# Optimization experiments

Hardware: AMD Instinct MI355X
Metric: run time of the kernel (lower is better)

## Reference

```python
import jax, jax.numpy as jnp
import numpy as np

EPS = 1e-08


def setup_inputs() -> dict:
    key = jax.random.key(0)
    k1, k2, k3 = jax.random.split(key, 3)
    N, IN_DIM, OUT_DIM = 8192, 512, 512
    h = jax.random.normal(k1, (N, IN_DIM), dtype=jnp.float32)
    adj = jax.random.randint(k2, (N, N), 0, 2, dtype=jnp.int32)
    # nn.Linear(in_dim, out_dim, bias=False) weight: [out_dim, in_dim]
    W = jax.random.normal(k3, (OUT_DIM, IN_DIM), dtype=jnp.float32) * (1.0 / np.sqrt(IN_DIM))
    return {"h": h, "adj": adj, "W": W}


def reference(h, adj, W):
    # Wh = h @ W^T  -> [N, out_dim]
    Wh = h @ W.T
    N = Wh.shape[0]
    norms = jnp.linalg.norm(Wh, axis=1, keepdims=True)  # [N, 1]
    # cosine similarity [N, N]
    sim = (Wh @ Wh.T) / (norms * norms.T + EPS)
    mask = (adj > 0) | jnp.eye(N, dtype=bool)
    sim_masked = jnp.where(mask, sim, -jnp.inf)
    alpha = jax.nn.softmax(sim_masked, axis=1)
    return alpha @ Wh
```

## Files before the change

kernel.cpp:

```cpp
#include <hip/hip_runtime.h>
#include <hip/hip_bf16.h>
#include <stdint.h>

#define NN 8192
#define DD 512

typedef unsigned short u16;
typedef __attribute__((ext_vector_type(8))) short short8;
typedef __attribute__((ext_vector_type(4))) float f32x4;

__device__ __forceinline__ void gld_lds16(const void* g, void* l) {
  __builtin_amdgcn_global_load_lds(
      (const __attribute__((address_space(1))) uint32_t*)(uintptr_t)g,
      (__attribute__((address_space(3))) uint32_t*)(uintptr_t)l,
      16, 0, 0);
}

__device__ __forceinline__ u16 f2bf(float f) {
  __hip_bfloat16 b = __float2bfloat16(f);
  return __builtin_bit_cast(u16, b);
}

__global__ void fill_kernel(float* __restrict__ p, int n, float v) {
  int i = blockIdx.x * 256 + threadIdx.x;
  int stride = gridDim.x * 256;
  for (; i < n; i += stride) p[i] = v;
}

__global__ void cvt4_kernel(const float4* __restrict__ src, ushort4* __restrict__ dst, int n4) {
  int i = blockIdx.x * 256 + threadIdx.x;
  int stride = gridDim.x * 256;
  for (; i < n4; i += stride) {
    float4 v = src[i];
    ushort4 o;
    o.x = f2bf(v.x); o.y = f2bf(v.y); o.z = f2bf(v.z); o.w = f2bf(v.w);
    dst[i] = o;
  }
}

__global__ void rownorm_kernel(const float* __restrict__ Wh, float* __restrict__ invn,
                               float* __restrict__ den) {
  int row = blockIdx.x;
  int l = threadIdx.x;
  const float4* p = (const float4*)(Wh + (size_t)row * DD);
  float4 a = p[l], b = p[l + 64];
  float s = a.x*a.x + a.y*a.y + a.z*a.z + a.w*a.w
          + b.x*b.x + b.y*b.y + b.z*b.z + b.w*b.w;
  #pragma unroll
  for (int off = 32; off; off >>= 1) s += __shfl_down(s, off);
  if (l == 0) {
    invn[row] = 1.0f / sqrtf(s);
    den[row] = 0.0f;
  }
}

__global__ void u_wht_kernel(const float* __restrict__ Wh, const float* __restrict__ invn,
                             u16* __restrict__ U, u16* __restrict__ WhT) {
  __shared__ float tile[64][65];
  int i0 = blockIdx.x * 64, d0 = blockIdx.y * 64;
  int c = threadIdx.x & 63, rb = threadIdx.x >> 6;
  #pragma unroll
  for (int r = rb; r < 64; r += 4) {
    float v = Wh[(size_t)(i0 + r) * DD + d0 + c];
    tile[r][c] = v;
    U[(size_t)(i0 + r) * DD + d0 + c] = f2bf(v * invn[i0 + r]);
  }
  __syncthreads();
  #pragma unroll
  for (int r = rb; r < 64; r += 4) {
    WhT[(size_t)(d0 + r) * NN + i0 + c] = f2bf(tile[c][r]);
  }
}

__global__ void __launch_bounds__(256) gemm_wh(
    const u16* __restrict__ A, const u16* __restrict__ B,
    int Nn, int K, float* __restrict__ Cf)
{
  __shared__ __align__(16) u16 As[128 * 32];
  __shared__ __align__(16) u16 Bs[128 * 32];

  const int tid = threadIdx.x;
  const int w = tid >> 6;
  const int lane = tid & 63;
  const int lm = lane & 15;
  const int q = lane >> 4;
  const int row0 = blockIdx.y * 128;
  const int col0 = blockIdx.x * 128;
  const int RM = (w >> 1) * 64;
  const int RN = (w & 1) * 64;
  const int sr = tid >> 2;
  const int sk = (tid & 3) * 8;

  f32x4 acc[4][4];
  #pragma unroll
  for (int a_ = 0; a_ < 4; a_++)
    #pragma unroll
    for (int b_ = 0; b_ < 4; b_++)
      acc[a_][b_] = (f32x4){0.f, 0.f, 0.f, 0.f};

  const size_t Abase = (size_t)row0 * K;
  const size_t Bbase = (size_t)col0 * K;

  for (int k0 = 0; k0 < K; k0 += 32) {
    __syncthreads();
    gld_lds16(A + Abase + (size_t)sr * K + k0 + sk,        (char*)As + w * 1024);
    gld_lds16(A + Abase + (size_t)(sr + 64) * K + k0 + sk, (char*)As + 4096 + w * 1024);
    gld_lds16(B + Bbase + (size_t)sr * K + k0 + sk,        (char*)Bs + w * 1024);
    gld_lds16(B + Bbase + (size_t)(sr + 64) * K + k0 + sk, (char*)Bs + 4096 + w * 1024);
    __syncthreads();

    short8 af[4], bfr[4];
    #pragma unroll
    for (int mt = 0; mt < 4; mt++)
      af[mt] = *(const short8*)&As[(RM + mt * 16 + lm) * 32 + q * 8];
    #pragma unroll
    for (int nt = 0; nt < 4; nt++)
      bfr[nt] = *(const short8*)&Bs[(RN + nt * 16 + lm) * 32 + q * 8];

    #pragma unroll
    for (int mt = 0; mt < 4; mt++)
      #pragma unroll
      for (int nt = 0; nt < 4; nt++)
        acc[mt][nt] = __builtin_amdgcn_mfma_f32_16x16x32_bf16(af[mt], bfr[nt], acc[mt][nt], 0, 0, 0);
  }

  #pragma unroll
  for (int mt = 0; mt < 4; mt++) {
    const int ib = row0 + RM + mt * 16 + q * 4;
    #pragma unroll
    for (int rr = 0; rr < 4; rr++) {
      const int i = ib + rr;
      #pragma unroll
      for (int nt = 0; nt < 4; nt++) {
        const int jc = col0 + RN + nt * 16 + lm;
        Cf[(size_t)i * Nn + jc] = acc[mt][nt][rr];
      }
    }
  }
}

__global__ void __launch_bounds__(512, 4) gemm_sim(
    const u16* __restrict__ U, const int* __restrict__ adj,
    u16* __restrict__ Pb, float* __restrict__ den)
{
  __shared__ __align__(16) char lds[49152];

  const int bj = blockIdx.x;
  const int bi = blockIdx.y;

  const int tid = threadIdx.x;
  const int w = tid >> 6;
  const int lane = tid & 63;
  const int lm = lane & 15;
  const int q = lane >> 4;
  const int row0 = bi * 256;
  const int col0 = bj * 128;
  const int wm = w >> 1;
  const int wn = w & 1;

  const u16* Ab = U + (size_t)row0 * DD;
  const u16* Bb = U + (size_t)col0 * DD;

  const int srow = tid >> 2;
  const int sch8 = (((tid & 3) ^ ((tid >> 3) & 3)) << 3);
  const int wofs = w << 10;

  const int rA = wm * 64 + lm;
  const int rB = wn * 64 + lm;
  const int aoff = rA * 64 + ((q ^ ((rA >> 1) & 3)) << 4);
  const int boff = 16384 + rB * 64 + ((q ^ ((rB >> 1) & 3)) << 4);

  f32x4 acc[4][4];
  #pragma unroll
  for (int a_ = 0; a_ < 4; a_++)
    #pragma unroll
    for (int b_ = 0; b_ < 4; b_++)
      acc[a_][b_] = (f32x4){0.f, 0.f, 0.f, 0.f};

  int na0[4][4], na1[4][4];
  {
    const int ib0 = row0 + wm * 64 + q * 4;
    #pragma unroll
    for (int rr = 0; rr < 4; rr++)
      #pragma unroll
      for (int nt = 0; nt < 4; nt++)
        na0[rr][nt] = adj[(size_t)(ib0 + rr) * NN + col0 + wn * 64 + nt * 16 + lm];
  }
  asm volatile("" ::: "memory");

#define SSTAGE(koff, dstoff)                                                      \
  do {                                                                            \
    char* d_ = lds + (dstoff);                                                    \
    gld_lds16(Ab + (size_t)srow * DD + (koff) + sch8,         d_ + wofs);         \
    gld_lds16(Ab + (size_t)(srow + 128) * DD + (koff) + sch8, d_ + 8192 + wofs);  \
    gld_lds16(Bb + (size_t)srow * DD + (koff) + sch8,         d_ + 16384 + wofs); \
  } while (0)

  SSTAGE(0, 0);
  SSTAGE(32, 24576);
  asm volatile("s_waitcnt vmcnt(3)" ::: "memory");
  asm volatile("s_barrier" ::: "memory");

#define STILE(T, CBOFF)                                                           \
  do {                                                                            \
    const char* cb = lds + (CBOFF);                                               \
    short8 af[4], bfr[4];                                                         \
    _Pragma("unroll")                                                             \
    for (int m = 0; m < 4; m++)                                                   \
      af[m] = *(const short8*)(cb + aoff + m * 1024);                             \
    _Pragma("unroll")                                                             \
    for (int n = 0; n < 4; n++)                                                   \
      bfr[n] = *(const short8*)(cb + boff + n * 1024);                            \
    asm volatile("s_barrier" ::: "memory");                                       \
    asm volatile("s_waitcnt lgkmcnt(0)" ::: "memory");                            \
    __builtin_amdgcn_s_setprio(1);                                                \
    _Pragma("unroll")                                                             \
    for (int m = 0; m < 2; m++)                                                   \
      _Pragma("unroll")                                                           \
      for (int n = 0; n < 4; n++)                                                 \
        acc[m][n] = __builtin_amdgcn_mfma_f32_16x16x32_bf16(af[m], bfr[n], acc[m][n], 0, 0, 0); \
    __builtin_amdgcn_s_setprio(0);                                                \
    asm volatile("s_barrier" ::: "memory");                                       \
    if ((T) + 2 < 16) SSTAGE(((T) + 2) * 32, CBOFF);                              \
    asm volatile("s_barrier" ::: "memory");                                       \
    __builtin_amdgcn_s_setprio(1);                                                \
    _Pragma("unroll")                                                             \
    for (int m = 2; m < 4; m++)                                                   \
      _Pragma("unroll")                                                           \
      for (int n = 0; n < 4; n++)                                                 \
        acc[m][n] = __builtin_amdgcn_mfma_f32_16x16x32_bf16(af[m], bfr[n], acc[m][n], 0, 0, 0); \
    __builtin_amdgcn_s_setprio(0);                                                \
    if ((T) + 2 < 16) { asm volatile("s_waitcnt vmcnt(3)" ::: "memory"); }        \
    else              { asm volatile("s_waitcnt vmcnt(0)" ::: "memory"); }        \
    asm volatile("s_barrier" ::: "memory");                                       \
  } while (0)

  #pragma unroll 1
  for (int t = 0; t < 16; t += 2) {
    STILE(t, 0);
    STILE(t + 1, 24576);
  }
#undef STILE
#undef SSTAGE

#define EPI(MT, NAC, NAN, DOLOAD)                                                 \
  do {                                                                            \
    if (DOLOAD) {                                                                 \
      const int ibn = row0 + wm * 64 + ((MT) + 1) * 16 + q * 4;                   \
      _Pragma("unroll")                                                           \
      for (int rr = 0; rr < 4; rr++)                                              \
        _Pragma("unroll")                                                         \
        for (int nt = 0; nt < 4; nt++)                                            \
          NAN[rr][nt] = adj[(size_t)(ibn + rr) * NN + col0 + wn * 64 + nt * 16 + lm]; \
    }                                                                             \
    const int ibc = row0 + wm * 64 + (MT) * 16 + q * 4;                           \
    _Pragma("unroll")                                                             \
    for (int rr = 0; rr < 4; rr++) {                                              \
      const int i = ibc + rr;                                                     \
      float psum = 0.f;                                                           \
      _Pragma("unroll")                                                           \
      for (int nt = 0; nt < 4; nt++) {                                            \
        const int jc = col0 + wn * 64 + nt * 16 + lm;                             \
        const float ev = __expf(acc[MT][nt][rr]);                                 \
        const bool on = (NAC[rr][nt] != 0) || (i == jc);                          \
        const float p = on ? ev : 0.0f;                                           \
        psum += p;                                                                \
        Pb[(size_t)i * NN + jc] = f2bf(p);                                        \
      }                                                                           \
      _Pragma("unroll")                                                           \
      for (int off = 8; off; off >>= 1) psum += __shfl_down(psum, off, 16);       \
      if (lm == 0) atomicAdd(&den[i], psum);                                      \
    }                                                                             \
  } while (0)

  EPI(0, na0, na1, 1);
  EPI(1, na1, na0, 1);
  EPI(2, na0, na1, 1);
  EPI(3, na1, na0, 0);
#undef EPI
}

__global__ void __launch_bounds__(512, 2) gemm_out2(
    const u16* __restrict__ P_,
    const u16* __restrict__ Wt,
    u16* __restrict__ p0, u16* __restrict__ p1,
    u16* __restrict__ p2, u16* __restrict__ p3)
{
  __shared__ __align__(16) char lds[65536];

  const int tid = threadIdx.x;
  const int lane = tid & 63;
  const int lm = lane & 15;
  const int q = lane >> 4;
  const int w = tid >> 6;
  const int wm = w >> 2;
  const int wn = w & 3;
  const int row0 = blockIdx.x * 256;
  const int col0 = blockIdx.y * 256;
  const int z = blockIdx.z;
  const int kBegin = z * (NN / 4);
  const int NT = (NN / 4) / 32;

  const u16* Ab = P_ + (size_t)row0 * NN;
  const u16* Bb = Wt + (size_t)col0 * NN;

  const int srow = tid >> 2;
  const int sch8 = (((tid & 3) ^ ((tid >> 3) & 3)) << 3);
  const int wofs = (tid >> 6) << 10;

  const int rA = wm * 128 + lm;
  const int rB = wn * 64 + lm;
  const int aoff = rA * 64 + ((q ^ ((rA >> 1) & 3)) << 4);
  const int boff = 16384 + rB * 64 + ((q ^ ((rB >> 1) & 3)) << 4);

  f32x4 acc[8][4];
  #pragma unroll
  for (int m = 0; m < 8; m++)
    #pragma unroll
    for (int n = 0; n < 4; n++)
      acc[m][n] = (f32x4){0.f, 0.f, 0.f, 0.f};

#define STAGE4(koff, dstoff)                                                      \
  do {                                                                            \
    char* d_ = lds + (dstoff);                                                    \
    gld_lds16(Ab + (size_t)srow * NN + (koff) + sch8,         d_ + wofs);         \
    gld_lds16(Ab + (size_t)(srow + 128) * NN + (koff) + sch8, d_ + 8192 + wofs);  \
    gld_lds16(Bb + (size_t)srow * NN + (koff) + sch8,         d_ + 16384 + wofs); \
    gld_lds16(Bb + (size_t)(srow + 128) * NN + (koff) + sch8, d_ + 24576 + wofs); \
  } while (0)

  STAGE4(kBegin, 0);
  STAGE4(kBegin + 32, 32768);
  asm volatile("s_waitcnt vmcnt(4)" ::: "memory");
  asm volatile("s_barrier" ::: "memory");

#define TILE(T, CBOFF)                                                            \
  do {                                                                            \
    const char* cb = lds + (CBOFF);                                               \
    short8 af[8], bf_[4];                                                         \
    _Pragma("unroll")                                                             \
    for (int m = 0; m < 8; m++)                                                   \
      af[m] = *(const short8*)(cb + aoff + m * 1024);                             \
    _Pragma("unroll")                                                             \
    for (int n = 0; n < 4; n++)                                                   \
      bf_[n] = *(const short8*)(cb + boff + n * 1024);                            \
    asm volatile("s_barrier" ::: "memory");                                       \
    asm volatile("s_waitcnt lgkmcnt(0)" ::: "memory");                            \
    __builtin_amdgcn_s_setprio(1);                                                \
    _Pragma("unroll")                                                             \
    for (int m = 0; m < 4; m++)                                                   \
      _Pragma("unroll")                                                           \
      for (int n = 0; n < 4; n++)                                                 \
        acc[m][n] = __builtin_amdgcn_mfma_f32_16x16x32_bf16(af[m], bf_[n], acc[m][n], 0, 0, 0); \
    __builtin_amdgcn_s_setprio(0);                                                \
    asm volatile("s_barrier" ::: "memory");                                       \
    if ((T) + 2 < NT) STAGE4(kBegin + ((T) + 2) * 32, CBOFF);                     \
    asm volatile("s_barrier" ::: "memory");                                       \
    __builtin_amdgcn_s_setprio(1);                                                \
    _Pragma("unroll")                                                             \
    for (int m = 4; m < 8; m++)                                                   \
      _Pragma("unroll")                                                           \
      for (int n = 0; n < 4; n++)                                                 \
        acc[m][n] = __builtin_amdgcn_mfma_f32_16x16x32_bf16(af[m], bf_[n], acc[m][n], 0, 0, 0); \
    __builtin_amdgcn_s_setprio(0);                                                \
    if ((T) + 2 < NT) { asm volatile("s_waitcnt vmcnt(4)" ::: "memory"); }        \
    else              { asm volatile("s_waitcnt vmcnt(0)" ::: "memory"); }        \
    asm volatile("s_barrier" ::: "memory");                                       \
  } while (0)

  #pragma unroll 1
  for (int t = 0; t < NT; t += 2) {
    TILE(t, 0);
    TILE(t + 1, 32768);
  }
#undef TILE
#undef STAGE4

  u16* const part = (z == 0) ? p0 : (z == 1) ? p1 : (z == 2) ? p2 : p3;
  #pragma unroll
  for (int m = 0; m < 8; m++) {
    const int ib = row0 + wm * 128 + m * 16 + q * 4;
    #pragma unroll
    for (int rr = 0; rr < 4; rr++) {
      const int i = ib + rr;
      #pragma unroll
      for (int n = 0; n < 4; n++) {
        const int dc = col0 + wn * 64 + n * 16 + lm;
        part[(size_t)i * DD + dc] = f2bf(acc[m][n][rr]);
      }
    }
  }
}

__global__ void reduce4_kernel(const uint4* __restrict__ p0, const uint4* __restrict__ p1,
                               const uint4* __restrict__ p2, const uint4* __restrict__ p3,
                               const float* __restrict__ den, float4* __restrict__ out) {
  const int idx = blockIdx.x * 256 + threadIdx.x;
  const int row = idx >> 6;
  const float dinv = 1.0f / den[row];
  float s[8] = {0, 0, 0, 0, 0, 0, 0, 0};
  #pragma unroll
  for (int zp = 0; zp < 4; zp++) {
    const uint4 u = (zp == 0 ? p0 : zp == 1 ? p1 : zp == 2 ? p2 : p3)[idx];
    s[0] += __uint_as_float(u.x << 16); s[1] += __uint_as_float(u.x & 0xffff0000u);
    s[2] += __uint_as_float(u.y << 16); s[3] += __uint_as_float(u.y & 0xffff0000u);
    s[4] += __uint_as_float(u.z << 16); s[5] += __uint_as_float(u.z & 0xffff0000u);
    s[6] += __uint_as_float(u.w << 16); s[7] += __uint_as_float(u.w & 0xffff0000u);
  }
  float4 o0 = {s[0] * dinv, s[1] * dinv, s[2] * dinv, s[3] * dinv};
  float4 o1 = {s[4] * dinv, s[5] * dinv, s[6] * dinv, s[7] * dinv};
  out[idx * 2] = o0;
  out[idx * 2 + 1] = o1;
}

extern "C" void kernel_launch(void* const* d_in, const int* in_sizes, int n_in,
                              void* d_out, int out_size, void* d_ws, size_t ws_size,
                              hipStream_t stream) {
  const float* h = (const float*)d_in[0];
  const int* adj = (const int*)d_in[1];
  const float* W = (const float*)d_in[2];
  float* out = (float*)d_out;

  const size_t SZ_P    = (size_t)NN * NN * 2;
  const size_t SZ_X0   = (size_t)NN * NN / 8;
  const size_t SZ_WHT  = (size_t)DD * NN * 2;
  const size_t SZ_HB   = (size_t)NN * DD * 2;
  const size_t SZ_WB   = (size_t)DD * DD * 2;
  const size_t SZ_U    = (size_t)NN * DD * 2;
  const size_t SZ_P3   = (size_t)NN * DD * 2;
  const size_t NEEDED  = SZ_P + SZ_X0 + SZ_WHT + SZ_HB + SZ_WB + SZ_U + SZ_P3 + 2 * (size_t)NN * 4;

  if (ws_size < NEEDED) {
    fill_kernel<<<256, 256, 0, stream>>>(out, out_size, 12345.0f);
    return;
  }

  char* ws = (char*)d_ws;
  size_t off = 0;
  u16*   P    = (u16*)(ws + off); off += SZ_P;
  u16*   x0   = (u16*)(ws + off); off += SZ_X0;
  u16*   WhT  = (u16*)(ws + off); off += SZ_WHT;
  u16*   hb   = (u16*)(ws + off); off += SZ_HB;
  u16*   Wb   = (u16*)(ws + off); off += SZ_WB;
  u16*   U    = (u16*)(ws + off); off += SZ_U;
  u16*   p3   = (u16*)(ws + off); off += SZ_P3;
  float* invn = (float*)(ws + off);
  float* den  = invn + NN;

  float* Wh = (float*)P;
  u16* part0 = x0;
  u16* part1 = U;
  u16* part2 = hb;
  u16* part3 = p3;

  cvt4_kernel<<<1024, 256, 0, stream>>>((const float4*)h, (ushort4*)hb, NN * DD / 4);
  cvt4_kernel<<<256, 256, 0, stream>>>((const float4*)W, (ushort4*)Wb, DD * DD / 4);
  gemm_wh<<<dim3(DD / 128, NN / 128), 256, 0, stream>>>(hb, Wb, DD, DD, Wh);
  rownorm_kernel<<<NN, 64, 0, stream>>>(Wh, invn, den);
  u_wht_kernel<<<dim3(NN / 64, DD / 64), 256, 0, stream>>>(Wh, invn, U, WhT);
  gemm_sim<<<dim3(NN / 128, NN / 256), 512, 0, stream>>>(U, adj, P, den);
  gemm_out2<<<dim3(NN / 256, DD / 256, 4), 512, 0, stream>>>(P, WhT, part0, part1, part2, part3);
  reduce4_kernel<<<NN * DD / 8 / 256, 256, 0, stream>>>(
      (const uint4*)part0, (const uint4*)part1, (const uint4*)part2, (const uint4*)part3,
      den, (float4*)out);
}
```

Measured before the change: 576.7 us.

## Fuse similarity, masking, exp and output GEMM into a flash-style kernel

Replaces the separate similarity GEMM (which wrote the full NxN bf16 probability matrix to global memory) and the split-K output GEMM with one flash-attention-style kernel. Each block keeps a 64-row Q tile in registers, streams K tiles and Wh^T tiles through LDS, computes exp with the adjacency mask into an LDS P tile, and accumulates P@Wh directly. The key range is split in two halves whose fp32 partials are summed by a lighter reduce kernel. This removes the large P round-trip through HBM, at the cost of a 144KB LDS footprint, high register pressure from 32 Q fragments held per thread, and only 256 blocks of occupancy.

```diff
diff --git a/kernel.cpp b/kernel.cpp
--- a/kernel.cpp
+++ b/kernel.cpp
@@ -139,278 +139,226 @@
   }
 }
 
-__global__ void __launch_bounds__(512, 4) gemm_sim(
-    const u16* __restrict__ U, const int* __restrict__ adj,
-    u16* __restrict__ Pb, float* __restrict__ den)
+__global__ void __launch_bounds__(512, 2) flash(
+    const u16* __restrict__ U,
+    const u16* __restrict__ Wt,
+    const int* __restrict__ adj,
+    float* __restrict__ accH,
+    float* __restrict__ den)
 {
-  __shared__ __align__(16) char lds[49152];
-
-  const int bj = blockIdx.x;
-  const int bi = blockIdx.y;
+  __shared__ __align__(16) char lds[147456];
+  constexpr int KV0 = 0, KV1 = 32768, WT0 = 65536, WT1 = 98304, POFF = 131072;
 
   const int tid = threadIdx.x;
   const int w = tid >> 6;
   const int lane = tid & 63;
   const int lm = lane & 15;
   const int q = lane >> 4;
-  const int row0 = bi * 256;
-  const int col0 = bj * 128;
-  const int wm = w >> 1;
-  const int wn = w & 1;
-
-  const u16* Ab = U + (size_t)row0 * DD;
-  const u16* Bb = U + (size_t)col0 * DD;
-
-  const int srow = tid >> 2;
-  const int sch8 = (((tid & 3) ^ ((tid >> 3) & 3)) << 3);
-  const int wofs = w << 10;
-
-  const int rA = wm * 64 + lm;
-  const int rB = wn * 64 + lm;
-  const int aoff = rA * 64 + ((q ^ ((rA >> 1) & 3)) << 4);
-  const int boff = 16384 + rB * 64 + ((q ^ ((rB >> 1) & 3)) << 4);
-
-  f32x4 acc[4][4];
-  #pragma unroll
-  for (int a_ = 0; a_ < 4; a_++)
-    #pragma unroll
-    for (int b_ = 0; b_ < 4; b_++)
-      acc[a_][b_] = (f32x4){0.f, 0.f, 0.f, 0.f};
-
-  int na0[4][4], na1[4][4];
+  const int rg = w >> 2;
+  const int xg = w & 3;
+  const int jh = blockIdx.x;
+  const int i0 = blockIdx.y * 64;
+  const int jb = jh * (NN / 2);
+  float* accP = accH + (size_t)jh * NN * DD;
+
+  const int kvrow = tid >> 4;
+  const int kvsrc = ((tid & 15) ^ (((tid >> 4) & 7) << 1)) * 8;
+  const int wtrow = tid >> 2;
+  const int wtsrc = ((tid & 3) ^ ((tid >> 3) & 3)) * 8;
+  const int sdst = w << 10;
+  const int sk_x = (lm & 7) << 1;
+  const int wq_x = (q ^ ((lm >> 1) & 3)) << 4;
+
+  f32x4 acc_s0[2], acc_s1[2], acc_o0[8], acc_o1[8];
+  #pragma unroll
+  for (int n = 0; n < 2; n++) { acc_s0[n] = (f32x4){0.f,0.f,0.f,0.f}; acc_s1[n] = (f32x4){0.f,0.f,0.f,0.f}; }
+  #pragma unroll
+  for (int n = 0; n < 8; n++) { acc_o0[n] = (f32x4){0.f,0.f,0.f,0.f}; acc_o1[n] = (f32x4){0.f,0.f,0.f,0.f}; }
+  float dacc0[4] = {0.f,0.f,0.f,0.f}, dacc1[4] = {0.f,0.f,0.f,0.f};
+  int na0[2][4], na1[2][4];
+
+  short8 Qf0[16], Qf1[16];
   {
-    const int ib0 = row0 + wm * 64 + q * 4;
-    #pragma unroll
-    for (int rr = 0; rr < 4; rr++)
-      #pragma unroll
-      for (int nt = 0; nt < 4; nt++)
-        na0[rr][nt] = adj[(size_t)(ib0 + rr) * NN + col0 + wn * 64 + nt * 16 + lm];
+    const u16* q0 = U + (size_t)(i0 + rg * 32 + lm) * DD + q * 8;
+    const u16* q1 = q0 + 16 * DD;
+    #pragma unroll
+    for (int ks = 0; ks < 16; ks++) {
+      Qf0[ks] = *(const short8*)(q0 + ks * 32);
+      Qf1[ks] = *(const short8*)(q1 + ks * 32);
+    }
   }
   asm volatile("" ::: "memory");
 
-#define SSTAGE(koff, dstoff)                                                      \
-  do {                                                                            \
-    char* d_ = lds + (dstoff);                                                    \
-    gld_lds16(Ab + (size_t)srow * DD + (koff) + sch8,         d_ + wofs);         \
-    gld_lds16(Ab + (size_t)(srow + 128) * DD + (koff) + sch8, d_ + 8192 + wofs);  \
-    gld_lds16(Bb + (size_t)srow * DD + (koff) + sch8,         d_ + 16384 + wofs); \
-  } while (0)
-
-  SSTAGE(0, 0);
-  SSTAGE(32, 24576);
-  asm volatile("s_waitcnt vmcnt(3)" ::: "memory");
+#define ADJ_LOAD(T_) do {                                                         \
+    const int* ap_ = adj + (size_t)(i0 + rg * 32 + q * 4) * NN + jb               \
+                     + (size_t)(T_) * 128 + xg * 32 + lm;                         \
+    _Pragma("unroll")                                                             \
+    for (int rr_ = 0; rr_ < 4; rr_++) {                                           \
+      na0[0][rr_] = ap_[(size_t)rr_ * NN];                                        \
+      na0[1][rr_] = ap_[(size_t)rr_ * NN + 16];                                   \
+      na1[0][rr_] = ap_[(size_t)(16 + rr_) * NN];                                 \
+      na1[1][rr_] = ap_[(size_t)(16 + rr_) * NN + 16];                            \
+    }                                                                             \
+  } while (0)
+
+#define STG_KV(T_, k0_, buf_) do {                                                \
+    const u16* s_ = U + (size_t)(jb + (T_) * 128 + kvrow) * DD + (k0_) + kvsrc;   \
+    gld_lds16(s_,             lds + (buf_) + sdst);                               \
+    gld_lds16(s_ + 32 * DD,   lds + (buf_) + 8192 + sdst);                        \
+    gld_lds16(s_ + 64 * DD,   lds + (buf_) + 16384 + sdst);                       \
+    gld_lds16(s_ + 96 * DD,   lds + (buf_) + 24576 + sdst);                       \
+  } while (0)
+
+#define STG_WT(T_, j2_, buf_) do {                                                \
+    const u16* s_ = Wt + (size_t)wtrow * NN + jb + (T_) * 128 + (j2_) * 32 + wtsrc; \
+    gld_lds16(s_,              lds + (buf_) + sdst);                              \
+    gld_lds16(s_ + 128 * NN,   lds + (buf_) + 8192 + sdst);                       \
+    gld_lds16(s_ + 256 * NN,   lds + (buf_) + 16384 + sdst);                      \
+    gld_lds16(s_ + 384 * NN,   lds + (buf_) + 24576 + sdst);                      \
+  } while (0)
+
+  ADJ_LOAD(0);
+  asm volatile("" ::: "memory");
+  STG_KV(0, 0, KV0);
+  STG_KV(0, 128, KV1);
+  asm volatile("s_waitcnt vmcnt(4)" ::: "memory");
   asm volatile("s_barrier" ::: "memory");
 
-#define STILE(T, CBOFF)                                                           \
-  do {                                                                            \
-    const char* cb = lds + (CBOFF);                                               \
-    short8 af[4], bfr[4];                                                         \
-    _Pragma("unroll")                                                             \
-    for (int m = 0; m < 4; m++)                                                   \
-      af[m] = *(const short8*)(cb + aoff + m * 1024);                             \
-    _Pragma("unroll")                                                             \
-    for (int n = 0; n < 4; n++)                                                   \
-      bfr[n] = *(const short8*)(cb + boff + n * 1024);                            \
+#define SSTEP(s_, buf_, STAGE_STMT, VMC) do {                                     \
+    short8 bn0_[4], bn1_[4];                                                      \
+    const char* cb_ = lds + (buf_);                                               \
+    _Pragma("unroll")                                                             \
+    for (int ks_ = 0; ks_ < 4; ks_++) {                                           \
+      bn0_[ks_] = *(const short8*)(cb_ + (xg * 32 + lm) * 256 + (((ks_ * 4 + q) ^ sk_x) << 4)); \
+      bn1_[ks_] = *(const short8*)(cb_ + (xg * 32 + 16 + lm) * 256 + (((ks_ * 4 + q) ^ sk_x) << 4)); \
+    }                                                                             \
     asm volatile("s_barrier" ::: "memory");                                       \
     asm volatile("s_waitcnt lgkmcnt(0)" ::: "memory");                            \
     __builtin_amdgcn_s_setprio(1);                                                \
     _Pragma("unroll")                                                             \
-    for (int m = 0; m < 2; m++)                                                   \
-      _Pragma("unroll")                                                           \
-      for (int n = 0; n < 4; n++)                                                 \
-        acc[m][n] = __builtin_amdgcn_mfma_f32_16x16x32_bf16(af[m], bfr[n], acc[m][n], 0, 0, 0); \
+    for (int ks_ = 0; ks_ < 4; ks_++) {                                           \
+      acc_s0[0] = __builtin_amdgcn_mfma_f32_16x16x32_bf16(Qf0[(s_) * 4 + ks_], bn0_[ks_], acc_s0[0], 0, 0, 0); \
+      acc_s0[1] = __builtin_amdgcn_mfma_f32_16x16x32_bf16(Qf0[(s_) * 4 + ks_], bn1_[ks_], acc_s0[1], 0, 0, 0); \
+      acc_s1[0] = __builtin_amdgcn_mfma_f32_16x16x32_bf16(Qf1[(s_) * 4 + ks_], bn0_[ks_], acc_s1[0], 0, 0, 0); \
+      acc_s1[1] = __builtin_amdgcn_mfma_f32_16x16x32_bf16(Qf1[(s_) * 4 + ks_], bn1_[ks_], acc_s1[1], 0, 0, 0); \
+    }                                                                             \
     __builtin_amdgcn_s_setprio(0);                                                \
     asm volatile("s_barrier" ::: "memory");                                       \
-    if ((T) + 2 < 16) SSTAGE(((T) + 2) * 32, CBOFF);                              \
-    asm volatile("s_barrier" ::: "memory");                                       \
-    __builtin_amdgcn_s_setprio(1);                                                \
-    _Pragma("unroll")                                                             \
-    for (int m = 2; m < 4; m++)                                                   \
-      _Pragma("unroll")                                                           \
-      for (int n = 0; n < 4; n++)                                                 \
-        acc[m][n] = __builtin_amdgcn_mfma_f32_16x16x32_bf16(af[m], bfr[n], acc[m][n], 0, 0, 0); \
-    __builtin_amdgcn_s_setprio(0);                                                \
-    if ((T) + 2 < 16) { asm volatile("s_waitcnt vmcnt(3)" ::: "memory"); }        \
-    else              { asm volatile("s_waitcnt vmcnt(0)" ::: "memory"); }        \
-    asm volatile("s_barrier" ::: "memory");                                       \
-  } while (0)
-
-  #pragma unroll 1
-  for (int t = 0; t < 16; t += 2) {
-    STILE(t, 0);
-    STILE(t + 1, 24576);
-  }
-#undef STILE
-#undef SSTAGE
-
-#define EPI(MT, NAC, NAN, DOLOAD)                                                 \
-  do {                                                                            \
-    if (DOLOAD) {                                                                 \
-      const int ibn = row0 + wm * 64 + ((MT) + 1) * 16 + q * 4;                   \
-      _Pragma("unroll")                                                           \
-      for (int rr = 0; rr < 4; rr++)                                              \
-        _Pragma("unroll")                                                         \
-        for (int nt = 0; nt < 4; nt++)                                            \
-          NAN[rr][nt] = adj[(size_t)(ibn + rr) * NN + col0 + wn * 64 + nt * 16 + lm]; \
-    }                                                                             \
-    const int ibc = row0 + wm * 64 + (MT) * 16 + q * 4;                           \
-    _Pragma("unroll")                                                             \
-    for (int rr = 0; rr < 4; rr++) {                                              \
-      const int i = ibc + rr;                                                     \
-      float psum = 0.f;                                                           \
-      _Pragma("unroll")                                                           \
-      for (int nt = 0; nt < 4; nt++) {                                            \
-        const int jc = col0 + wn * 64 + nt * 16 + lm;                             \
-        const float ev = __expf(acc[MT][nt][rr]);                                 \
-        const bool on = (NAC[rr][nt] != 0) || (i == jc);                          \
-        const float p = on ? ev : 0.0f;                                           \
-        psum += p;                                                                \
-        Pb[(size_t)i * NN + jc] = f2bf(p);                                        \
-      }                                                                           \
-      _Pragma("unroll")                                                           \
-      for (int off = 8; off; off >>= 1) psum += __shfl_down(psum, off, 16);       \
-      if (lm == 0) atomicAdd(&den[i], psum);                                      \
-    }                                                                             \
-  } while (0)
-
-  EPI(0, na0, na1, 1);
-  EPI(1, na1, na0, 1);
-  EPI(2, na0, na1, 1);
-  EPI(3, na1, na0, 0);
-#undef EPI
-}
-
-__global__ void __launch_bounds__(512, 2) gemm_out2(
-    const u16* __restrict__ P_,
-    const u16* __restrict__ Wt,
-    u16* __restrict__ p0, u16* __restrict__ p1,
-    u16* __restrict__ p2, u16* __restrict__ p3)
-{
-  __shared__ __align__(16) char lds[65536];
-
-  const int tid = threadIdx.x;
-  const int lane = tid & 63;
-  const int lm = lane & 15;
-  const int q = lane >> 4;
-  const int w = tid >> 6;
-  const int wm = w >> 2;
-  const int wn = w & 3;
-  const int row0 = blockIdx.x * 256;
-  const int col0 = blockIdx.y * 256;
-  const int z = blockIdx.z;
-  const int kBegin = z * (NN / 4);
-  const int NT = (NN / 4) / 32;
-
-  const u16* Ab = P_ + (size_t)row0 * NN;
-  const u16* Bb = Wt + (size_t)col0 * NN;
-
-  const int srow = tid >> 2;
-  const int sch8 = (((tid & 3) ^ ((tid >> 3) & 3)) << 3);
-  const int wofs = (tid >> 6) << 10;
-
-  const int rA = wm * 128 + lm;
-  const int rB = wn * 64 + lm;
-  const int aoff = rA * 64 + ((q ^ ((rA >> 1) & 3)) << 4);
-  const int boff = 16384 + rB * 64 + ((q ^ ((rB >> 1) & 3)) << 4);
-
-  f32x4 acc[8][4];
-  #pragma unroll
-  for (int m = 0; m < 8; m++)
-    #pragma unroll
-    for (int n = 0; n < 4; n++)
-      acc[m][n] = (f32x4){0.f, 0.f, 0.f, 0.f};
-
-#define STAGE4(koff, dstoff)                                                      \
-  do {                                                                            \
-    char* d_ = lds + (dstoff);                                                    \
-    gld_lds16(Ab + (size_t)srow * NN + (koff) + sch8,         d_ + wofs);         \
-    gld_lds16(Ab + (size_t)(srow + 128) * NN + (koff) + sch8, d_ + 8192 + wofs);  \
-    gld_lds16(Bb + (size_t)srow * NN + (koff) + sch8,         d_ + 16384 + wofs); \
-    gld_lds16(Bb + (size_t)(srow + 128) * NN + (koff) + sch8, d_ + 24576 + wofs); \
-  } while (0)
-
-  STAGE4(kBegin, 0);
-  STAGE4(kBegin + 32, 32768);
-  asm volatile("s_waitcnt vmcnt(4)" ::: "memory");
-  asm volatile("s_barrier" ::: "memory");
-
-#define TILE(T, CBOFF)                                                            \
-  do {                                                                            \
-    const char* cb = lds + (CBOFF);                                               \
-    short8 af[8], bf_[4];                                                         \
-    _Pragma("unroll")                                                             \
-    for (int m = 0; m < 8; m++)                                                   \
-      af[m] = *(const short8*)(cb + aoff + m * 1024);                             \
-    _Pragma("unroll")                                                             \
-    for (int n = 0; n < 4; n++)                                                   \
-      bf_[n] = *(const short8*)(cb + boff + n * 1024);                            \
+    STAGE_STMT;                                                                   \
+    asm volatile("s_waitcnt " VMC ::: "memory");                                  \
+    asm volatile("s_barrier" ::: "memory");                                       \
+  } while (0)
+
+#define PSTEP(p_, buf_, STAGE_STMT, POST_STMT, VMC) do {                          \
+    short8 pa0_, pa1_, wb_[8];                                                    \
+    pa0_ = *(const short8*)(lds + POFF + (rg * 32 + lm) * 256 + ((((p_) * 4 + q) ^ sk_x) << 4)); \
+    pa1_ = *(const short8*)(lds + POFF + (rg * 32 + 16 + lm) * 256 + ((((p_) * 4 + q) ^ sk_x) << 4)); \
+    const char* wbb_ = lds + (buf_);                                              \
+    _Pragma("unroll")                                                             \
+    for (int nt_ = 0; nt_ < 8; nt_++)                                             \
+      wb_[nt_] = *(const short8*)(wbb_ + (xg * 128 + nt_ * 16 + lm) * 64 + wq_x); \
     asm volatile("s_barrier" ::: "memory");                                       \
     asm volatile("s_waitcnt lgkmcnt(0)" ::: "memory");                            \
     __builtin_amdgcn_s_setprio(1);                                                \
     _Pragma("unroll")                                                             \
-    for (int m = 0; m < 4; m++)                                                   \
+    for (int nt_ = 0; nt_ < 8; nt_++) {                                           \
+      acc_o0[nt_] = __builtin_amdgcn_mfma_f32_16x16x32_bf16(pa0_, wb_[nt_], acc_o0[nt_], 0, 0, 0); \
+      acc_o1[nt_] = __builtin_amdgcn_mfma_f32_16x16x32_bf16(pa1_, wb_[nt_], acc_o1[nt_], 0, 0, 0); \
+    }                                                                             \
+    __builtin_amdgcn_s_setprio(0);                                                \
+    asm volatile("s_barrier" ::: "memory");                                       \
+    STAGE_STMT;                                                                   \
+    asm volatile("s_waitcnt " VMC ::: "memory");                                  \
+    POST_STMT;                                                                    \
+    asm volatile("s_barrier" ::: "memory");                                       \
+  } while (0)
+
+#define ESTEP(T_) do {                                                            \
+    _Pragma("unroll")                                                             \
+    for (int nt_ = 0; nt_ < 2; nt_++) {                                           \
       _Pragma("unroll")                                                           \
-      for (int n = 0; n < 4; n++)                                                 \
-        acc[m][n] = __builtin_amdgcn_mfma_f32_16x16x32_bf16(af[m], bf_[n], acc[m][n], 0, 0, 0); \
-    __builtin_amdgcn_s_setprio(0);                                                \
-    asm volatile("s_barrier" ::: "memory");                                       \
-    if ((T) + 2 < NT) STAGE4(kBegin + ((T) + 2) * 32, CBOFF);                     \
-    asm volatile("s_barrier" ::: "memory");                                       \
-    __builtin_amdgcn_s_setprio(1);                                                \
-    _Pragma("unroll")                                                             \
-    for (int m = 4; m < 8; m++)                                                   \
-      _Pragma("unroll")                                                           \
-      for (int n = 0; n < 4; n++)                                                 \
-        acc[m][n] = __builtin_amdgcn_mfma_f32_16x16x32_bf16(af[m], bf_[n], acc[m][n], 0, 0, 0); \
-    __builtin_amdgcn_s_setprio(0);                                                \
-    if ((T) + 2 < NT) { asm volatile("s_waitcnt vmcnt(4)" ::: "memory"); }        \
-    else              { asm volatile("s_waitcnt vmcnt(0)" ::: "memory"); }        \
+      for (int rr_ = 0; rr_ < 4; rr_++) {                                         \
+        const int col_ = xg * 32 + nt_ * 16 + lm;                                 \
+        const int jc_ = jb + (T_) * 128 + col_;                                   \
+        {                                                                         \
+          const int i_ = i0 + rg * 32 + q * 4 + rr_;                              \
+          const float ev_ = __expf(acc_s0[nt_][rr_]);                             \
+          const float p_ = (na0[nt_][rr_] != 0 || i_ == jc_) ? ev_ : 0.0f;        \
+          dacc0[rr_] += p_;                                                       \
+          const int rp_ = rg * 32 + q * 4 + rr_;                                  \
+          *(u16*)(lds + POFF + rp_ * 256 + ((((col_ >> 3) ^ ((rp_ & 7) << 1)) << 4)) + (col_ & 7) * 2) = f2bf(p_); \
+        }                                                                         \
+        {                                                                         \
+          const int i_ = i0 + rg * 32 + 16 + q * 4 + rr_;                         \
+          const float ev_ = __expf(acc_s1[nt_][rr_]);                             \
+          const float p_ = (na1[nt_][rr_] != 0 || i_ == jc_) ? ev_ : 0.0f;        \
+          dacc1[rr_] += p_;                                                       \
+          const int rp_ = rg * 32 + 16 + q * 4 + rr_;                             \
+          *(u16*)(lds + POFF + rp_ * 256 + ((((col_ >> 3) ^ ((rp_ & 7) << 1)) << 4)) + (col_ & 7) * 2) = f2bf(p_); \
+        }                                                                         \
+      }                                                                           \
+      acc_s0[nt_] = (f32x4){0.f, 0.f, 0.f, 0.f};                                  \
+      acc_s1[nt_] = (f32x4){0.f, 0.f, 0.f, 0.f};                                  \
+    }                                                                             \
+    asm volatile("s_waitcnt lgkmcnt(0)" ::: "memory");                            \
     asm volatile("s_barrier" ::: "memory");                                       \
   } while (0)
 
   #pragma unroll 1
-  for (int t = 0; t < NT; t += 2) {
-    TILE(t, 0);
-    TILE(t + 1, 32768);
-  }
-#undef TILE
-#undef STAGE4
-
-  u16* const part = (z == 0) ? p0 : (z == 1) ? p1 : (z == 2) ? p2 : p3;
-  #pragma unroll
-  for (int m = 0; m < 8; m++) {
-    const int ib = row0 + wm * 128 + m * 16 + q * 4;
+  for (int T = 0; T < 32; T++) {
+    SSTEP(0, KV0, STG_KV(T, 256, KV0), "vmcnt(4)");
+    SSTEP(1, KV1, STG_KV(T, 384, KV1), "vmcnt(4)");
+    SSTEP(2, KV0, STG_WT(T, 0, WT0), "vmcnt(4)");
+    SSTEP(3, KV1, STG_WT(T, 1, WT1), "vmcnt(4)");
+    ESTEP(T);
+    PSTEP(0, WT0, STG_WT(T, 2, WT0), {}, "vmcnt(4)");
+    PSTEP(1, WT1, STG_WT(T, 3, WT1), {}, "vmcnt(4)");
+    if (T < 31) {
+      PSTEP(2, WT0, STG_KV(T + 1, 0, KV0), ADJ_LOAD(T + 1), "vmcnt(4)");
+      PSTEP(3, WT1, STG_KV(T + 1, 128, KV1), {}, "vmcnt(20)");
+    } else {
+      PSTEP(2, WT0, {}, {}, "vmcnt(0)");
+      PSTEP(3, WT1, {}, {}, "vmcnt(0)");
+    }
+  }
+#undef SSTEP
+#undef PSTEP
+#undef ESTEP
+#undef STG_KV
+#undef STG_WT
+#undef ADJ_LOAD
+
+  #pragma unroll
+  for (int rr = 0; rr < 4; rr++) {
+    float s0 = dacc0[rr], s1 = dacc1[rr];
+    #pragma unroll
+    for (int off = 8; off; off >>= 1) {
+      s0 += __shfl_down(s0, off, 16);
+      s1 += __shfl_down(s1, off, 16);
+    }
+    if (lm == 0) {
+      atomicAdd(&den[i0 + rg * 32 + q * 4 + rr], s0);
+      atomicAdd(&den[i0 + rg * 32 + 16 + q * 4 + rr], s1);
+    }
+  }
+  #pragma unroll
+  for (int nt = 0; nt < 8; nt++) {
     #pragma unroll
     for (int rr = 0; rr < 4; rr++) {
-      const int i = ib + rr;
-      #pragma unroll
-      for (int n = 0; n < 4; n++) {
-        const int dc = col0 + wn * 64 + n * 16 + lm;
-        part[(size_t)i * DD + dc] = f2bf(acc[m][n][rr]);
-      }
-    }
-  }
-}
-
-__global__ void reduce4_kernel(const uint4* __restrict__ p0, const uint4* __restrict__ p1,
-                               const uint4* __restrict__ p2, const uint4* __restrict__ p3,
+      accP[(size_t)(i0 + rg * 32 + q * 4 + rr) * DD + xg * 128 + nt * 16 + lm] = acc_o0[nt][rr];
+      accP[(size_t)(i0 + rg * 32 + 16 + q * 4 + rr) * DD + xg * 128 + nt * 16 + lm] = acc_o1[nt][rr];
+    }
+  }
+}
+
+__global__ void reduce2_kernel(const float4* __restrict__ a0, const float4* __restrict__ a1,
                                const float* __restrict__ den, float4* __restrict__ out) {
   const int idx = blockIdx.x * 256 + threadIdx.x;
-  const int row = idx >> 6;
+  const int row = idx >> 7;
   const float dinv = 1.0f / den[row];
-  float s[8] = {0, 0, 0, 0, 0, 0, 0, 0};
-  #pragma unroll
-  for (int zp = 0; zp < 4; zp++) {
-    const uint4 u = (zp == 0 ? p0 : zp == 1 ? p1 : zp == 2 ? p2 : p3)[idx];
-    s[0] += __uint_as_float(u.x << 16); s[1] += __uint_as_float(u.x & 0xffff0000u);
-    s[2] += __uint_as_float(u.y << 16); s[3] += __uint_as_float(u.y & 0xffff0000u);
-    s[4] += __uint_as_float(u.z << 16); s[5] += __uint_as_float(u.z & 0xffff0000u);
-    s[6] += __uint_as_float(u.w << 16); s[7] += __uint_as_float(u.w & 0xffff0000u);
-  }
-  float4 o0 = {s[0] * dinv, s[1] * dinv, s[2] * dinv, s[3] * dinv};
-  float4 o1 = {s[4] * dinv, s[5] * dinv, s[6] * dinv, s[7] * dinv};
-  out[idx * 2] = o0;
-  out[idx * 2 + 1] = o1;
+  float4 x = a0[idx], y = a1[idx];
+  float4 o = {(x.x + y.x) * dinv, (x.y + y.y) * dinv, (x.z + y.z) * dinv, (x.w + y.w) * dinv};
+  out[idx] = o;
 }
 
 extern "C" void kernel_launch(void* const* d_in, const int* in_sizes, int n_in,
@@ -421,14 +369,12 @@
   const float* W = (const float*)d_in[2];
   float* out = (float*)d_out;
 
-  const size_t SZ_P    = (size_t)NN * NN * 2;
-  const size_t SZ_X0   = (size_t)NN * NN / 8;
-  const size_t SZ_WHT  = (size_t)DD * NN * 2;
-  const size_t SZ_HB   = (size_t)NN * DD * 2;
-  const size_t SZ_WB   = (size_t)DD * DD * 2;
-  const size_t SZ_U    = (size_t)NN * DD * 2;
-  const size_t SZ_P3   = (size_t)NN * DD * 2;
-  const size_t NEEDED  = SZ_P + SZ_X0 + SZ_WHT + SZ_HB + SZ_WB + SZ_U + SZ_P3 + 2 * (size_t)NN * 4;
+  const size_t SZ_ACC = (size_t)2 * NN * DD * 4;
+  const size_t SZ_WHT = (size_t)DD * NN * 2;
+  const size_t SZ_HB  = (size_t)NN * DD * 2;
+  const size_t SZ_WB  = (size_t)DD * DD * 2;
+  const size_t SZ_U   = (size_t)NN * DD * 2;
+  const size_t NEEDED = SZ_ACC + SZ_WHT + SZ_HB + SZ_WB + SZ_U + 2 * (size_t)NN * 4;
 
   if (ws_size < NEEDED) {
     fill_kernel<<<256, 256, 0, stream>>>(out, out_size, 12345.0f);
@@ -437,30 +383,23 @@
 
   char* ws = (char*)d_ws;
   size_t off = 0;
-  u16*   P    = (u16*)(ws + off); off += SZ_P;
-  u16*   x0   = (u16*)(ws + off); off += SZ_X0;
+  float* acc0 = (float*)(ws + off); off += SZ_ACC;
   u16*   WhT  = (u16*)(ws + off); off += SZ_WHT;
   u16*   hb   = (u16*)(ws + off); off += SZ_HB;
   u16*   Wb   = (u16*)(ws + off); off += SZ_WB;
   u16*   U    = (u16*)(ws + off); off += SZ_U;
-  u16*   p3   = (u16*)(ws + off); off += SZ_P3;
   float* invn = (float*)(ws + off);
   float* den  = invn + NN;
 
-  float* Wh = (float*)P;
-  u16* part0 = x0;
-  u16* part1 = U;
-  u16* part2 = hb;
-  u16* part3 = p3;
+  float* Wh = acc0;
+  float* acc1 = acc0 + (size_t)NN * DD;
 
   cvt4_kernel<<<1024, 256, 0, stream>>>((const float4*)h, (ushort4*)hb, NN * DD / 4);
   cvt4_kernel<<<256, 256, 0, stream>>>((const float4*)W, (ushort4*)Wb, DD * DD / 4);
   gemm_wh<<<dim3(DD / 128, NN / 128), 256, 0, stream>>>(hb, Wb, DD, DD, Wh);
   rownorm_kernel<<<NN, 64, 0, stream>>>(Wh, invn, den);
   u_wht_kernel<<<dim3(NN / 64, DD / 64), 256, 0, stream>>>(Wh, invn, U, WhT);
-  gemm_sim<<<dim3(NN / 128, NN / 256), 512, 0, stream>>>(U, adj, P, den);
-  gemm_out2<<<dim3(NN / 256, DD / 256, 4), 512, 0, stream>>>(P, WhT, part0, part1, part2, part3);
-  reduce4_kernel<<<NN * DD / 8 / 256, 256, 0, stream>>>(
-      (const uint4*)part0, (const uint4*)part1, (const uint4*)part2, (const uint4*)part3,
-      den, (float4*)out);
-}
+  flash<<<dim3(2, NN / 64), 512, 0, stream>>>(U, WhT, adj, acc0, den);
+  reduce2_kernel<<<NN * DD / 4 / 256, 256, 0, stream>>>(
+      (const float4*)acc0, (const float4*)acc1, den, (float4*)out);
+}
```

Result: slower. 1.209 ms (+109.5%).
